# Optimization experiments

Hardware: AMD Instinct MI355X
Metric: run time of the kernel (lower is better)

## Reference

```python
import jax, jax.numpy as jnp
import numpy as np
from jax import lax

N_EMBD = 1024
N_HEAD = 16
HEAD_DIM = N_EMBD // N_HEAD
EPS = 1e-6
B, T = 4, 2048


def setup_inputs() -> dict:
    key = jax.random.key(0)
    ks = jax.random.split(key, 5)
    scale = 1.0 / np.sqrt(N_EMBD)
    return {
        "x": jax.random.normal(ks[0], (B, T, N_EMBD), jnp.float32),
        "W_attn": jax.random.normal(ks[1], (N_EMBD, 3 * N_EMBD), jnp.float32) * scale,
        "b_attn": jax.random.normal(ks[2], (3 * N_EMBD,), jnp.float32) * 0.01,
        "W_proj": jax.random.normal(ks[3], (N_EMBD, N_EMBD), jnp.float32) * scale,
        "b_proj": jax.random.normal(ks[4], (N_EMBD,), jnp.float32) * 0.01,
    }


def _feature_map(x):
    # ELU + 1 for non-negativity
    return jax.nn.elu(x) + 1.0


def reference(x, W_attn, b_attn, W_proj, b_proj):
    Bb, Tt, C = x.shape
    qkv = x @ W_attn + b_attn  # (B,T,3C)
    q, k, v = jnp.split(qkv, 3, axis=-1)

    def to_heads(t):
        # (B,T,C) -> (T,B,H,d): scan axis leading
        return t.reshape(Bb, Tt, N_HEAD, HEAD_DIM).transpose(1, 0, 2, 3)

    q = _feature_map(to_heads(q))
    k = _feature_map(to_heads(k))
    v = to_heads(v)

    # Causal linear attention: O(d^2) running state instead of the torch
    # code's materialized (B,H,T,d,d) cumsum — same math.
    def step(carry, inp):
        kv, ksum = carry  # (B,H,d,d), (B,H,d)
        qt, kt, vt = inp  # each (B,H,d)
        kv = kv + kt[..., :, None] * vt[..., None, :]
        ksum = ksum + kt
        num = jnp.einsum('bhi,bhij->bhj', qt, kv)
        den = jnp.einsum('bhi,bhi->bh', qt, ksum)[..., None] + EPS
        return (kv, ksum), num / den

    init = (
        jnp.zeros((Bb, N_HEAD, HEAD_DIM, HEAD_DIM), x.dtype),
        jnp.zeros((Bb, N_HEAD, HEAD_DIM), x.dtype),
    )
    _, y = lax.scan(step, init, (q, k, v))  # (T,B,H,d)
    y = y.transpose(1, 0, 2, 3).reshape(Bb, Tt, C)
    return y @ W_proj + b_proj  # dropout is identity in eval mode
```

## Files before the change

### kernel.cpp

```cpp
#include <hip/hip_runtime.h>
#include <math.h>

#define BB   4
#define TT   2048
#define CC   1024
#define HH   16
#define DD   64
#define MM   (BB*TT)
#define NQKV (3*CC)
#define LCH  128
#define NCH  (TT/LCH)
#define EPSF 1e-6f

#define QKST 72
#define PST  136
#define VTST 136

typedef __bf16 bf16x8 __attribute__((ext_vector_type(8)));
typedef float  floatx4 __attribute__((ext_vector_type(4)));

__device__ __forceinline__ unsigned short f2bf(float f) {
  union { float f; unsigned int u; } v; v.f = f;
  unsigned int r = v.u + 0x7fffu + ((v.u >> 16) & 1u);
  return (unsigned short)(r >> 16);
}
__device__ __forceinline__ float bf2f(unsigned short s) {
  union { unsigned int u; float f; } v; v.u = ((unsigned int)s) << 16;
  return v.f;
}
__device__ __forceinline__ float featmap(float v) {
  return v > 0.f ? v + 1.f : __expf(v);
}
__device__ __forceinline__ void gld_lds_b128(const unsigned short* g, unsigned short* l) {
  __builtin_amdgcn_global_load_lds(
      (const __attribute__((address_space(1))) unsigned int*)g,
      (__attribute__((address_space(3))) unsigned int*)l, 16, 0, 0);
}


__global__ __launch_bounds__(256) void cvt_x_kernel(const float* __restrict__ x,
                                                    unsigned short* __restrict__ xb, int n) {
  int i = (blockIdx.x * 256 + threadIdx.x) * 4;
  if (i < n) {
    float4 f = *(const float4*)(x + i);
    ushort4 o;
    o.x = f2bf(f.x); o.y = f2bf(f.y); o.z = f2bf(f.z); o.w = f2bf(f.w);
    *(ushort4*)(xb + i) = o;
  }
}

__global__ __launch_bounds__(256) void transpose_cvt_kernel(const float* __restrict__ W,
                                                            unsigned short* __restrict__ out,
                                                            int R, int Cc) {
  __shared__ float tile[32][33];
  int bx = blockIdx.x * 32;
  int by = blockIdx.y * 32;
  int tx = threadIdx.x, ty = threadIdx.y;
  #pragma unroll
  for (int i = ty; i < 32; i += 8)
    tile[i][tx] = W[(size_t)(by + i) * Cc + bx + tx];
  __syncthreads();
  #pragma unroll
  for (int i = ty; i < 32; i += 8)
    out[(size_t)(bx + i) * R + by + tx] = f2bf(tile[tx][i]);
}

#define GEMM_K_LOOP(A_, Bt_, K_)                                                 \
  __shared__ __align__(16) unsigned short As[128 * 64];                          \
  __shared__ __align__(16) unsigned short Bs[128 * 64];                          \
  int tid = threadIdx.x;                                                         \
  int wave = tid >> 6, lane = tid & 63;                                          \
  int lr = lane & 15, lq = lane >> 4;                                            \
  int m0 = blockIdx.y * 128, n0 = blockIdx.x * 128;                              \
  int wm = (wave >> 1) * 64, wn = (wave & 1) * 64;                               \
  int lrow = lane >> 3;                        \
  int lk = (lane & 7) ^ lrow;                       \
  int rbase = wave * 32;                                                         \
  const unsigned short* gA = A_ + (size_t)(m0 + rbase + lrow) * K_ + lk * 8;     \
  const unsigned short* gB = Bt_ + (size_t)(n0 + rbase + lrow) * K_ + lk * 8;    \
  unsigned short* lA = As + rbase * 64;                                          \
  unsigned short* lB = Bs + rbase * 64;                                          \
  floatx4 acc[4][4] = {};                                                        \
  for (int k0 = 0; k0 < K_; k0 += 64) {                                          \
    __syncthreads();                 \
    _Pragma("unroll")                                                            \
    for (int g = 0; g < 4; g++) {                                                \
      gld_lds_b128(gA + k0 + (size_t)g * 8 * K_, lA + g * 512);                  \
      gld_lds_b128(gB + k0 + (size_t)g * 8 * K_, lB + g * 512);                  \
    }                                                                            \
    __syncthreads();                                    \
    _Pragma("unroll")                                                            \
    for (int kk = 0; kk < 2; kk++) {                                             \
      bf16x8 an[4], bm[4];                                                       \
      _Pragma("unroll")                                                          \
      for (int i = 0; i < 4; i++)                                                \
        an[i] = *(const bf16x8*)&Bs[(wn + i * 16 + lr) * 64 + ((((kk << 2) + lq) ^ (lr & 7)) << 3)]; \
      _Pragma("unroll")                                                          \
      for (int j = 0; j < 4; j++)                                                \
        bm[j] = *(const bf16x8*)&As[(wm + j * 16 + lr) * 64 + ((((kk << 2) + lq) ^ (lr & 7)) << 3)]; \
      _Pragma("unroll")                                                          \
      for (int i = 0; i < 4; i++)                                                \
        _Pragma("unroll")                                                        \
        for (int j = 0; j < 4; j++)                                              \
          acc[i][j] = __builtin_amdgcn_mfma_f32_16x16x32_bf16(an[i], bm[j], acc[i][j], 0, 0, 0); \
    }                                                                            \
  }

__global__ __launch_bounds__(256) void gemm_qkv_kernel(
    const unsigned short* __restrict__ A, const unsigned short* __restrict__ Bt,
    const float* __restrict__ bias,
    unsigned short* __restrict__ qh, unsigned short* __restrict__ kh,
    unsigned short* __restrict__ vh) {
  GEMM_K_LOOP(A, Bt, CC)
  int which = n0 >> 10;
  unsigned short* dst = (which == 0) ? qh : (which == 1) ? kh : vh;
  #pragma unroll
  for (int i = 0; i < 4; i++) {
    int n = n0 + wn + i * 16 + lq * 4;
    int h = (n & 1023) >> 6, dd = n & 63;
    float4 bi = *(const float4*)&bias[n];
    #pragma unroll
    for (int j = 0; j < 4; j++) {
      int m = m0 + wm + j * 16 + lr;
      int b = m >> 11, t = m & 2047;
      float v0 = acc[i][j][0] + bi.x, v1 = acc[i][j][1] + bi.y;
      float v2 = acc[i][j][2] + bi.z, v3 = acc[i][j][3] + bi.w;
      if (which < 2) { v0 = featmap(v0); v1 = featmap(v1); v2 = featmap(v2); v3 = featmap(v3); }
      ushort4 o; o.x = f2bf(v0); o.y = f2bf(v1); o.z = f2bf(v2); o.w = f2bf(v3);
      size_t idx = (((size_t)(b * HH + h)) * TT + t) * DD + dd;
      *(ushort4*)&dst[idx] = o;
    }
  }
}

__global__ __launch_bounds__(256) void gemm_proj_kernel(
    const unsigned short* __restrict__ A, const unsigned short* __restrict__ Bt,
    const float* __restrict__ bias, float* __restrict__ out) {
  GEMM_K_LOOP(A, Bt, CC)
  #pragma unroll
  for (int i = 0; i < 4; i++) {
    int n = n0 + wn + i * 16 + lq * 4;
    float4 bi = *(const float4*)&bias[n];
    #pragma unroll
    for (int j = 0; j < 4; j++) {
      int m = m0 + wm + j * 16 + lr;
      float4 o;
      o.x = acc[i][j][0] + bi.x; o.y = acc[i][j][1] + bi.y;
      o.z = acc[i][j][2] + bi.z; o.w = acc[i][j][3] + bi.w;
      *(float4*)&out[(size_t)m * CC + n] = o;
    }
  }
}

__global__ __launch_bounds__(256) void chunk_state_kernel(
    const unsigned short* __restrict__ kh, const unsigned short* __restrict__ vh,
    float* __restrict__ KVx) {
  __shared__ __align__(16) unsigned short Kt[64 * VTST];
  __shared__ __align__(16) unsigned short Vt[80 * VTST];
  int blk = blockIdx.x;
  int bh = blk / NCH, c = blk % NCH;
  int tid = threadIdx.x;
  const unsigned short* kp = kh + ((size_t)bh * TT + c * LCH) * DD;
  const unsigned short* vp = vh + ((size_t)bh * TT + c * LCH) * DD;
  {
    int t = tid & 127;
    for (int j8 = (tid >> 7) * 8; j8 < DD; j8 += 16) {
      union { uint4 u; unsigned short s[8]; } wk, wv;
      wk.u = *(const uint4*)&kp[(size_t)t * DD + j8];
      wv.u = *(const uint4*)&vp[(size_t)t * DD + j8];
      #pragma unroll
      for (int jj = 0; jj < 8; jj++) {
        Kt[(j8 + jj) * VTST + t] = wk.s[jj];
        Vt[(j8 + jj) * VTST + t] = wv.s[jj];
      }
    }
  }
  for (int e = tid; e < 16 * 128; e += 256) {
    int rr = e >> 7, n = e & 127;
    Vt[(64 + rr) * VTST + n] = (rr == 0) ? (unsigned short)0x3F80 : (unsigned short)0;
  }
  __syncthreads();
  int wave = tid >> 6, lane = tid & 63;
  int lr = lane & 15, lq = lane >> 4;
  int i0 = wave * 16;
  floatx4 acc[5] = {};
  #pragma unroll
  for (int kk = 0; kk < 4; kk++) {
    bf16x8 a = *(const bf16x8*)&Kt[(i0 + lr) * VTST + kk * 32 + lq * 8];
    #pragma unroll
    for (int jt = 0; jt < 5; jt++) {
      bf16x8 b = *(const bf16x8*)&Vt[(jt * 16 + lr) * VTST + kk * 32 + lq * 8];
      acc[jt] = __builtin_amdgcn_mfma_f32_16x16x32_bf16(a, b, acc[jt], 0, 0, 0);
    }
  }
  float* o = KVx + (size_t)blk * 5120;
  #pragma unroll
  for (int jt = 0; jt < 5; jt++)
    #pragma unroll
    for (int r = 0; r < 4; r++)
      o[(jt * 16 + lr) * 64 + i0 + lq * 4 + r] = acc[jt][r];
}

__global__ __launch_bounds__(256) void prefix_state_kernel(const float* __restrict__ KVx,
                                                           unsigned short* __restrict__ SPb) {
  int bh = blockIdx.x / 5, jb = blockIdx.x % 5;
  int e = jb * 1024 + threadIdx.x * 4;
  float run0 = 0.f, run1 = 0.f, run2 = 0.f, run3 = 0.f;
  for (int c = 0; c < NCH; c++) {
    size_t base = ((size_t)bh * NCH + c) * 5120 + e;
    float4 v = *(const float4*)&KVx[base];
    ushort4 o;
    o.x = f2bf(run0); o.y = f2bf(run1); o.z = f2bf(run2); o.w = f2bf(run3);
    *(ushort4*)&SPb[base] = o;
    run0 += v.x; run1 += v.y; run2 += v.z; run3 += v.w;
  }
}

__global__ __launch_bounds__(256) void chunk_attn_kernel(
    const unsigned short* __restrict__ qh, const unsigned short* __restrict__ kh,
    const unsigned short* __restrict__ vh, const unsigned short* __restrict__ SPb,
    unsigned short* __restrict__ yb) {
  __shared__ __align__(16) unsigned short lds[128 * QKST * 2 + 80 * VTST];
  unsigned short* Qs = lds;
  unsigned short* Ks = lds + 128 * QKST;
  unsigned short* P  = lds;
  unsigned short* Vt = lds + 128 * QKST * 2;

  int blk = blockIdx.x;
  int bh = blk / NCH, c = blk % NCH;
  int b = bh / HH, h = bh % HH;
  int tid = threadIdx.x;
  const unsigned short* qp = qh + ((size_t)bh * TT + c * LCH) * DD;
  const unsigned short* kp = kh + ((size_t)bh * TT + c * LCH) * DD;
  const unsigned short* vp = vh + ((size_t)bh * TT + c * LCH) * DD;

  for (int e = tid; e < 1024; e += 256) {
    int row = e >> 3, k8 = (e & 7) * 8;
    *(uint4*)&Qs[row * QKST + k8] = *(const uint4*)&qp[(size_t)row * DD + k8];
    *(uint4*)&Ks[row * QKST + k8] = *(const uint4*)&kp[(size_t)row * DD + k8];
  }
  {
    int t = tid & 127;
    for (int j8 = (tid >> 7) * 8; j8 < DD; j8 += 16) {
      union { uint4 u; unsigned short s[8]; } w;
      w.u = *(const uint4*)&vp[(size_t)t * DD + j8];
      #pragma unroll
      for (int jj = 0; jj < 8; jj++) Vt[(j8 + jj) * VTST + t] = w.s[jj];
    }
  }
  for (int e = tid; e < 16 * 128; e += 256) {
    int rr = e >> 7, n = e & 127;
    Vt[(64 + rr) * VTST + n] = (rr == 0) ? (unsigned short)0x3F80 : (unsigned short)0;
  }
  __syncthreads();

  int wave = tid >> 6, lane = tid & 63;
  int lr = lane & 15, lq = lane >> 4;
  int mbase = wave * 32;

  bf16x8 aq[2][2];
  #pragma unroll
  for (int i = 0; i < 2; i++)
    #pragma unroll
    for (int kk = 0; kk < 2; kk++)
      aq[i][kk] = *(const bf16x8*)&Qs[(mbase + i * 16 + lr) * QKST + kk * 32 + lq * 8];

  floatx4 acc[2][5] = {};
  const unsigned short* spb = SPb + (size_t)blk * (80 * 64);
  #pragma unroll
  for (int jt = 0; jt < 5; jt++)
    #pragma unroll
    for (int kk = 0; kk < 2; kk++) {
      bf16x8 bsp = *(const bf16x8*)&spb[(jt * 16 + lr) * 64 + kk * 32 + lq * 8];
      acc[0][jt] = __builtin_amdgcn_mfma_f32_16x16x32_bf16(aq[0][kk], bsp, acc[0][jt], 0, 0, 0);
      acc[1][jt] = __builtin_amdgcn_mfma_f32_16x16x32_bf16(aq[1][kk], bsp, acc[1][jt], 0, 0, 0);
    }
  floatx4 sacc[2][8] = {};
  #pragma unroll
  for (int nt = 0; nt < 8; nt++)
    #pragma unroll
    for (int kk = 0; kk < 2; kk++) {
      bf16x8 bk = *(const bf16x8*)&Ks[(nt * 16 + lr) * QKST + kk * 32 + lq * 8];
      sacc[0][nt] = __builtin_amdgcn_mfma_f32_16x16x32_bf16(aq[0][kk], bk, sacc[0][nt], 0, 0, 0);
      sacc[1][nt] = __builtin_amdgcn_mfma_f32_16x16x32_bf16(aq[1][kk], bk, sacc[1][nt], 0, 0, 0);
    }
  __syncthreads();

  #pragma unroll
  for (int i = 0; i < 2; i++)
    #pragma unroll
    for (int nt = 0; nt < 8; nt++) {
      int col = nt * 16 + lr;
      #pragma unroll
      for (int r = 0; r < 4; r++) {
        int m = mbase + i * 16 + lq * 4 + r;
        float v = (col <= m) ? sacc[i][nt][r] : 0.f;
        P[m * PST + col] = f2bf(v);
      }
    }
  __syncthreads();

  #pragma unroll
  for (int kk4 = 0; kk4 < 4; kk4++) {
    bf16x8 ap0 = *(const bf16x8*)&P[(mbase + lr) * PST + kk4 * 32 + lq * 8];
    bf16x8 ap1 = *(const bf16x8*)&P[(mbase + 16 + lr) * PST + kk4 * 32 + lq * 8];
    #pragma unroll
    for (int jt = 0; jt < 5; jt++) {
      bf16x8 bv = *(const bf16x8*)&Vt[(jt * 16 + lr) * VTST + kk4 * 32 + lq * 8];
      acc[0][jt] = __builtin_amdgcn_mfma_f32_16x16x32_bf16(ap0, bv, acc[0][jt], 0, 0, 0);
      acc[1][jt] = __builtin_amdgcn_mfma_f32_16x16x32_bf16(ap1, bv, acc[1][jt], 0, 0, 0);
    }
  }

  int srclane = lq << 4;
  #pragma unroll
  for (int i = 0; i < 2; i++) {
    #pragma unroll
    for (int r = 0; r < 4; r++) {
      float den = __shfl(acc[i][4][r], srclane, 64);
      float inv = 1.f / (den + EPSF);
      int tg = c * LCH + mbase + i * 16 + lq * 4 + r;
      size_t base = ((size_t)b * TT + tg) * CC + h * DD;
      #pragma unroll
      for (int jt = 0; jt < 4; jt++)
        yb[base + jt * 16 + lr] = f2bf(acc[i][jt][r] * inv);
    }
  }
}

extern "C" void kernel_launch(void* const* d_in, const int* in_sizes, int n_in,
                              void* d_out, int out_size, void* d_ws, size_t ws_size,
                              hipStream_t stream) {
  const float* x      = (const float*)d_in[0];
  const float* W_attn = (const float*)d_in[1];
  const float* b_attn = (const float*)d_in[2];
  const float* W_proj = (const float*)d_in[3];
  const float* b_proj = (const float*)d_in[4];
  float* out = (float*)d_out;

  char* ws = (char*)d_ws;
  size_t off = 0;
  auto alloc = [&](size_t bytes) -> char* {
    char* p = ws + off;
    off += (bytes + 255) & ~(size_t)255;
    return p;
  };
  unsigned short* xb  = (unsigned short*)alloc((size_t)MM * CC * 2);
  unsigned short* WaT = (unsigned short*)alloc((size_t)NQKV * CC * 2);
  unsigned short* WpT = (unsigned short*)alloc((size_t)CC * CC * 2);
  unsigned short* qh  = (unsigned short*)alloc((size_t)MM * CC * 2);
  unsigned short* kh  = (unsigned short*)alloc((size_t)MM * CC * 2);
  unsigned short* vh  = (unsigned short*)alloc((size_t)MM * CC * 2);
  float* KVx = (float*)alloc((size_t)BB * HH * NCH * 80 * 64 * 4);
  unsigned short* SPb = (unsigned short*)alloc((size_t)BB * HH * NCH * 80 * 64 * 2);
  unsigned short* yb = xb;

  cvt_x_kernel<<<(MM * CC) / 1024, 256, 0, stream>>>(x, xb, MM * CC);
  transpose_cvt_kernel<<<dim3(NQKV / 32, CC / 32), dim3(32, 8), 0, stream>>>(W_attn, WaT, CC, NQKV);
  transpose_cvt_kernel<<<dim3(CC / 32, CC / 32), dim3(32, 8), 0, stream>>>(W_proj, WpT, CC, CC);
  gemm_qkv_kernel<<<dim3(NQKV / 128, MM / 128), 256, 0, stream>>>(xb, WaT, b_attn, qh, kh, vh);
  chunk_state_kernel<<<BB * HH * NCH, 256, 0, stream>>>(kh, vh, KVx);
  prefix_state_kernel<<<BB * HH * 5, 256, 0, stream>>>(KVx, SPb);
  chunk_attn_kernel<<<BB * HH * NCH, 256, 0, stream>>>(qh, kh, vh, SPb, yb);
  gemm_proj_kernel<<<dim3(CC / 128, MM / 128), 256, 0, stream>>>(yb, WpT, b_proj, out);
}
```

Before: 240.9 us.

## Fuse preprocessing launches and load GEMM A operand directly from global memory

```diff
diff --git a/kernel.cpp b/kernel.cpp
--- a/kernel.cpp
+++ b/kernel.cpp
@@ -37,36 +37,42 @@
       (__attribute__((address_space(3))) unsigned int*)l, 16, 0, 0);
 }
 
-
-__global__ __launch_bounds__(256) void cvt_x_kernel(const float* __restrict__ x,
-                                                    unsigned short* __restrict__ xb, int n) {
-  int i = (blockIdx.x * 256 + threadIdx.x) * 4;
-  if (i < n) {
+__device__ __forceinline__ void transpose_cvt_body(const float* __restrict__ W,
+                                                   unsigned short* __restrict__ out,
+                                                   int R, int Cc, int bx32, int by32, int tid) {
+  __shared__ float tile[32][33];
+  int tx = tid & 31, ty = tid >> 5;
+  int bx = bx32 * 32, by = by32 * 32;
+  #pragma unroll
+  for (int i = ty; i < 32; i += 8)
+    tile[i][tx] = W[(size_t)(by + i) * Cc + bx + tx];
+  __syncthreads();
+  #pragma unroll
+  for (int i = ty; i < 32; i += 8)
+    out[(size_t)(bx + i) * R + by + tx] = f2bf(tile[tx][i]);
+}
+
+__global__ __launch_bounds__(256) void prep_kernel(
+    const float* __restrict__ x, unsigned short* __restrict__ xb,
+    const float* __restrict__ Wa, unsigned short* __restrict__ WaT,
+    const float* __restrict__ Wp, unsigned short* __restrict__ WpT) {
+  int blk = blockIdx.x, tid = threadIdx.x;
+  if (blk < 8192) {
+    int i = (blk * 256 + tid) * 4;
     float4 f = *(const float4*)(x + i);
     ushort4 o;
     o.x = f2bf(f.x); o.y = f2bf(f.y); o.z = f2bf(f.z); o.w = f2bf(f.w);
     *(ushort4*)(xb + i) = o;
-  }
-}
-
-__global__ __launch_bounds__(256) void transpose_cvt_kernel(const float* __restrict__ W,
-                                                            unsigned short* __restrict__ out,
-                                                            int R, int Cc) {
-  __shared__ float tile[32][33];
-  int bx = blockIdx.x * 32;
-  int by = blockIdx.y * 32;
-  int tx = threadIdx.x, ty = threadIdx.y;
-  #pragma unroll
-  for (int i = ty; i < 32; i += 8)
-    tile[i][tx] = W[(size_t)(by + i) * Cc + bx + tx];
-  __syncthreads();
-  #pragma unroll
-  for (int i = ty; i < 32; i += 8)
-    out[(size_t)(bx + i) * R + by + tx] = f2bf(tile[tx][i]);
+  } else if (blk < 8192 + 3072) {
+    int t = blk - 8192;
+    transpose_cvt_body(Wa, WaT, CC, NQKV, t % 96, t / 96, tid);
+  } else {
+    int t = blk - 11264;
+    transpose_cvt_body(Wp, WpT, CC, CC, t % 32, t / 32, tid);
+  }
 }
 
 #define GEMM_K_LOOP(A_, Bt_, K_)                                                 \
-  __shared__ __align__(16) unsigned short As[128 * 64];                          \
   __shared__ __align__(16) unsigned short Bs[128 * 64];                          \
   int tid = threadIdx.x;                                                         \
   int wave = tid >> 6, lane = tid & 63;                                          \
@@ -76,33 +82,33 @@
   int lrow = lane >> 3;                        \
   int lk = (lane & 7) ^ lrow;                       \
   int rbase = wave * 32;                                                         \
-  const unsigned short* gA = A_ + (size_t)(m0 + rbase + lrow) * K_ + lk * 8;     \
   const unsigned short* gB = Bt_ + (size_t)(n0 + rbase + lrow) * K_ + lk * 8;    \
-  unsigned short* lA = As + rbase * 64;                                          \
   unsigned short* lB = Bs + rbase * 64;                                          \
+  const unsigned short* gA = A_ + (size_t)(m0 + wm + lr) * K_ + lq * 8;          \
   floatx4 acc[4][4] = {};                                                        \
   for (int k0 = 0; k0 < K_; k0 += 64) {                                          \
-    __syncthreads();                 \
+    __syncthreads();               \
     _Pragma("unroll")                                                            \
-    for (int g = 0; g < 4; g++) {                                                \
-      gld_lds_b128(gA + k0 + (size_t)g * 8 * K_, lA + g * 512);                  \
+    for (int g = 0; g < 4; g++)                                                  \
       gld_lds_b128(gB + k0 + (size_t)g * 8 * K_, lB + g * 512);                  \
-    }                                                                            \
-    __syncthreads();                                    \
+    bf16x8 bm[2][4];                       \
+    _Pragma("unroll")                                                            \
+    for (int kk = 0; kk < 2; kk++)                                               \
+      _Pragma("unroll")                                                          \
+      for (int j = 0; j < 4; j++)                                                \
+        bm[kk][j] = *(const bf16x8*)&gA[k0 + kk * 32 + (size_t)j * 16 * K_];     \
+    __syncthreads();                                       \
     _Pragma("unroll")                                                            \
     for (int kk = 0; kk < 2; kk++) {                                             \
-      bf16x8 an[4], bm[4];                                                       \
+      bf16x8 an[4];                                                              \
       _Pragma("unroll")                                                          \
       for (int i = 0; i < 4; i++)                                                \
         an[i] = *(const bf16x8*)&Bs[(wn + i * 16 + lr) * 64 + ((((kk << 2) + lq) ^ (lr & 7)) << 3)]; \
       _Pragma("unroll")                                                          \
-      for (int j = 0; j < 4; j++)                                                \
-        bm[j] = *(const bf16x8*)&As[(wm + j * 16 + lr) * 64 + ((((kk << 2) + lq) ^ (lr & 7)) << 3)]; \
-      _Pragma("unroll")                                                          \
       for (int i = 0; i < 4; i++)                                                \
         _Pragma("unroll")                                                        \
         for (int j = 0; j < 4; j++)                                              \
-          acc[i][j] = __builtin_amdgcn_mfma_f32_16x16x32_bf16(an[i], bm[j], acc[i][j], 0, 0, 0); \
+          acc[i][j] = __builtin_amdgcn_mfma_f32_16x16x32_bf16(an[i], bm[kk][j], acc[i][j], 0, 0, 0); \
     }                                                                            \
   }
 
@@ -355,9 +361,7 @@
   unsigned short* SPb = (unsigned short*)alloc((size_t)BB * HH * NCH * 80 * 64 * 2);
   unsigned short* yb = xb;
 
-  cvt_x_kernel<<<(MM * CC) / 1024, 256, 0, stream>>>(x, xb, MM * CC);
-  transpose_cvt_kernel<<<dim3(NQKV / 32, CC / 32), dim3(32, 8), 0, stream>>>(W_attn, WaT, CC, NQKV);
-  transpose_cvt_kernel<<<dim3(CC / 32, CC / 32), dim3(32, 8), 0, stream>>>(W_proj, WpT, CC, CC);
+  prep_kernel<<<12288, 256, 0, stream>>>(x, xb, W_attn, WaT, W_proj, WpT);
   gemm_qkv_kernel<<<dim3(NQKV / 128, MM / 128), 256, 0, stream>>>(xb, WaT, b_attn, qh, kh, vh);
   chunk_state_kernel<<<BB * HH * NCH, 256, 0, stream>>>(kh, vh, KVx);
   prefix_state_kernel<<<BB * HH * 5, 256, 0, stream>>>(KVx, SPb);
```

New measurement: 302.9 us. 1.26x slower.
